# Optimization experiments

Hardware: AMD Instinct MI355X
Metric: run time of the kernel (lower is better)

The kernel has to match this reference:

```python
import jax, jax.numpy as jnp
import numpy as np
from jax.scipy.linalg import solve_triangular

B = 131072; OBS = 128; AD = 8; H = 64; FH = 32; NL = 4
D1 = AD // 2; D2 = AD - D1; TRIL = AD * (AD + 1) // 2
_rows, _cols = np.tril_indices(AD)          # same row-major order as torch.tril_indices
_diag = (_rows == _cols)                    # bool mask over TRIL entries
_diag_pos = np.where(_diag)[0]
LOG2PI = float(np.log(2.0 * np.pi))
EPS = float(np.finfo(np.float32).eps)       # torch RMSNorm default eps = finfo.eps


def _rms(x, w):
    return x * jax.lax.rsqrt(jnp.mean(x * x, axis=-1, keepdims=True) + EPS) * w


def setup_inputs() -> dict:
    ks = iter(jax.random.split(jax.random.key(0), 32))
    def w(shape, scale):
        return jax.random.normal(next(ks), shape, jnp.float32) * scale
    z = lambda *s: jnp.zeros(s, jnp.float32)
    return dict(
        x=jax.random.normal(next(ks), (B, OBS), jnp.float32),
        action=jax.random.normal(next(ks), (B, AD), jnp.float32),
        z_rpo=jax.random.uniform(next(ks), (B, AD), jnp.float32, -0.1, 0.1),
        cW1=w((OBS, H), OBS ** -0.5), cb1=z(H), c_rms=jnp.ones(H, jnp.float32),
        cW2=w((H, H), H ** -0.5), cb2=z(H), cW3=w((H, 1), H ** -0.5), cb3=z(1),
        aW1=w((OBS, H), OBS ** -0.5), ab1=z(H), aW2=w((H, H), H ** -0.5), ab2=z(H),
        mW=w((H, AD), 0.01), mb=z(AD),
        tW1=w((OBS, H), OBS ** -0.5), tb1=z(H), t_rms1=jnp.ones(H, jnp.float32),
        tW2=w((H, H), H ** -0.5), tb2=z(H), t_rms2=jnp.ones(H, jnp.float32),
        hW=w((H, TRIL), 0.01), hb=z(TRIL),
        fW1=w((NL, D1 + OBS, FH), (D1 + OBS) ** -0.5), fb1=z(NL, FH),
        fW2=w((NL, FH, 2 * D2), 0.01), fb2=z(NL, 2 * D2),
    )


def reference(x, action, z_rpo, cW1, cb1, c_rms, cW2, cb2, cW3, cb3,
              aW1, ab1, aW2, ab2, mW, mb,
              tW1, tb1, t_rms1, tW2, tb2, t_rms2, hW, hb,
              fW1, fb1, fW2, fb2):
    silu = jax.nn.silu
    Bn = x.shape[0]
    # actor mean trunk + head, with RPO uniform perturbation (action is given)
    h = silu(silu(x @ aW1 + ab1) @ aW2 + ab2)
    action_mean = h @ mW + mb + z_rpo
    # state-dependent lower-triangular covariance factor
    tl = _rms(silu(x @ tW1 + tb1), t_rms1)
    tl = _rms(silu(tl @ tW2 + tb2), t_rms2)
    raw = tl @ hW + hb                                   # [B, TRIL]
    proc = jnp.where(_diag, jax.nn.softplus(raw), raw)
    L = jnp.zeros((Bn, AD, AD), raw.dtype).at[:, _rows, _cols].set(proc)
    log_det_L = jnp.log(proc[:, _diag_pos]).sum(-1)      # [B]
    # coupling flow inverse: noise -> correlated
    noise = action - action_mean
    x1, x2 = noise[:, :D1], noise[:, D1:]
    fld = jnp.zeros((Bn,), raw.dtype)
    for i in reversed(range(NL)):
        cond, y = (x1, x2) if i % 2 == 0 else (x2, x1)
        st = silu(jnp.concatenate([cond, x], -1) @ fW1[i] + fb1[i]) @ fW2[i] + fb2[i]
        s_raw, tshift = jnp.split(st, 2, -1)
        s = jnp.tanh(s_raw) * 2.0
        xt = (y - tshift) * jnp.exp(-s)
        if i % 2 == 0:
            x2 = xt
        else:
            x1 = xt
        fld = fld + s.sum(-1)
    correlated = jnp.concatenate([x1, x2], -1)           # [B, AD]
    zc = solve_triangular(L, correlated[..., None], lower=True)[..., 0]
    mahal = (zc * zc).sum(-1)
    log_prob = -0.5 * (AD * LOG2PI + mahal) - log_det_L - fld
    entropy = 0.5 * (AD * (1.0 + LOG2PI)) + log_det_L + fld
    # critic
    v = _rms(silu(x @ cW1 + cb1), c_rms)
    v = silu(v @ cW2 + cb2) @ cW3 + cb3                  # [B, 1]
    return (action, log_prob, entropy, v)
```

## Files before the change

### kernel.cpp

```cpp
#include <hip/hip_runtime.h>

typedef __attribute__((ext_vector_type(8))) short    v8s;
typedef __attribute__((ext_vector_type(4))) float    f4;
typedef __attribute__((ext_vector_type(2))) float    f2;
typedef __attribute__((ext_vector_type(2))) unsigned u32x2;

#define MFMA16 __builtin_amdgcn_mfma_f32_16x16x32_bf16

#define AW1T 0
#define TW1T 8192
#define CW1T 16384
#define AW2T 24576
#define TW2T 28672
#define CW2T 32768
#define MWT  36864
#define HWT  37888
#define FW1XT 40960
#define FW2T  57344
#define WS_BF16_TOTAL 59392
#define W1CTO 0
#define HBPO  512

#define LOG2PI 1.83787706640934548356f
#define EPSF   1.1920928955078125e-07f

__device__ __constant__ int PERM[36] = {0,2,5,9,14,20,27,35,
  1,3,4,6,7,8,10,11,12,13,15,16,17,18,19,21,22,23,24,25,26,28,29,30,31,32,33,34};

__device__ __forceinline__ float ubits(unsigned u){union{unsigned u;float f;}c;c.u=u;return c.f;}
__device__ __forceinline__ unsigned fbits(float f){union{float f;unsigned u;}c;c.f=f;return c.u;}
__device__ __forceinline__ float rcpf(float x){ return __builtin_amdgcn_rcpf(x); }
__device__ __forceinline__ float siluf(float v){ return v * rcpf(1.f + __expf(-v)); }
__device__ __forceinline__ unsigned pk2(float a,float b){
  unsigned ua=fbits(a); ua+=0x7fffu+((ua>>16)&1u);
  unsigned ub=fbits(b); ub+=0x7fffu+((ub>>16)&1u);
  return (ua>>16)|(ub&0xffff0000u);
}
__device__ __forceinline__ unsigned short f2bu(float a){
  unsigned ua=fbits(a); ua+=0x7fffu+((ua>>16)&1u);
  return (unsigned short)(ua>>16);
}
__device__ __forceinline__ float b2f16(unsigned short h){ return ubits(((unsigned)h)<<16); }
__device__ __forceinline__ float qsum(float v){
  v += __shfl_xor(v,16,64); v += __shfl_xor(v,32,64); return v;
}
__device__ __forceinline__ int swz(int row, int blk){ return row*64 + ((blk ^ (row&7))*8); }

__global__ __launch_bounds__(256)
void prep_kernel(const float* __restrict__ aW1, const float* __restrict__ aW2,
                 const float* __restrict__ mW,  const float* __restrict__ tW1,
                 const float* __restrict__ tW2, const float* __restrict__ hW,
                 const float* __restrict__ hb,  const float* __restrict__ cW1,
                 const float* __restrict__ cW2, const float* __restrict__ fW1,
                 const float* __restrict__ fW2,
                 unsigned short* __restrict__ ws16, float* __restrict__ wsf)
{
  const int tid = blockIdx.x*256 + threadIdx.x;
  const int stride = gridDim.x*256;
  for (int idx=tid; idx<64*128; idx+=stride){
    int n=idx>>7, k=idx&127;
    ws16[AW1T+idx]=f2bu(aW1[k*64+n]);
    ws16[TW1T+idx]=f2bu(tW1[k*64+n]);
    ws16[CW1T+idx]=f2bu(cW1[k*64+n]);
  }
  for (int idx=tid; idx<64*64; idx+=stride){
    int n=idx>>6, k=idx&63;
    ws16[AW2T+idx]=f2bu(aW2[k*64+n]);
    ws16[TW2T+idx]=f2bu(tW2[k*64+n]);
    ws16[CW2T+idx]=f2bu(cW2[k*64+n]);
  }
  for (int idx=tid; idx<16*64; idx+=stride){
    int n=idx>>6, k=idx&63;
    ws16[MWT+idx]=f2bu(n<8 ? mW[k*8+n] : 0.f);
  }
  for (int idx=tid; idx<48*64; idx+=stride){
    int n=idx>>6, k=idx&63;
    ws16[HWT+idx]=f2bu(n<36 ? hW[k*36+PERM[n]] : 0.f);
  }
  for (int idx=tid; idx<4*32*128; idx+=stride){
    int i=idx>>12, rem=idx&4095, n=rem>>7, k=rem&127;
    ws16[FW1XT+idx]=f2bu(fW1[i*4224 + (4+k)*32 + n]);
  }
  for (int idx=tid; idx<4*16*32; idx+=stride){
    int i=idx>>9, rem=idx&511, n=rem>>5, k=rem&31;
    ws16[FW2T+idx]=f2bu(n<8 ? fW2[i*256 + k*8 + n] : 0.f);
  }
  for (int idx=tid; idx<4*32*4; idx+=stride){
    int i=idx>>7, rem=idx&127, n=rem>>2, k=rem&3;
    wsf[W1CTO+idx]=fW1[i*4224 + k*32 + n];
  }
  for (int idx=tid; idx<48; idx+=stride)
    wsf[HBPO+idx] = idx<36 ? hb[PERM[idx]] : 0.f;
}

template<int NWT>
__device__ __forceinline__ void gemmX(const unsigned short* __restrict__ Wt,
                                      const v8s* __restrict__ xf,
                                      f4 (*acc)[2], int c, int q)
{
#pragma unroll
  for (int kt=0; kt<4; ++kt){
    v8s wf[NWT];
#pragma unroll
    for (int wt=0; wt<NWT; ++wt)
      wf[wt] = *(const v8s*)(Wt + (wt*16 + c)*128 + kt*32 + q*8);
#pragma unroll
    for (int wt=0; wt<NWT; ++wt)
#pragma unroll
      for (int et=0; et<2; ++et)
        acc[wt][et] = MFMA16(wf[wt], xf[et*4+kt], acc[wt][et], 0,0,0);
  }
}

template<int NWT>
__device__ __forceinline__ void gemmH(const unsigned short* __restrict__ Wt,
                                      const unsigned short* __restrict__ actL,
                                      f4 (*acc)[2], int c, int q)
{
#pragma unroll
  for (int kt=0; kt<2; ++kt){
    v8s wf[NWT];
#pragma unroll
    for (int wt=0; wt<NWT; ++wt)
      wf[wt] = *(const v8s*)(Wt + (wt*16 + c)*64 + kt*32 + q*8);
    v8s af[2];
#pragma unroll
    for (int et=0; et<2; ++et)
      af[et] = *(const v8s*)(actL + swz(et*16+c, kt*4+q));
#pragma unroll
    for (int wt=0; wt<NWT; ++wt)
#pragma unroll
      for (int et=0; et<2; ++et)
        acc[wt][et] = MFMA16(wf[wt], af[et], acc[wt][et], 0,0,0);
  }
}

__global__ __launch_bounds__(64) __attribute__((amdgpu_waves_per_eu(3, 4)))
void policy_kernel(
    const float* __restrict__ x,    const float* __restrict__ action, const float* __restrict__ z_rpo,
    const float* __restrict__ cb1,  const float* __restrict__ c_rms,  const float* __restrict__ cb2,
    const float* __restrict__ cW3,  const float* __restrict__ cb3,
    const float* __restrict__ ab1,  const float* __restrict__ ab2,    const float* __restrict__ mb,
    const float* __restrict__ tb1,  const float* __restrict__ t_rms1, const float* __restrict__ tb2,
    const float* __restrict__ t_rms2,
    const float* __restrict__ fb1,  const float* __restrict__ fb2,
    const unsigned short* __restrict__ ws16, const float* __restrict__ wsf,
    float* __restrict__ out, const int Btot)
{
  const int lane = threadIdx.x;
  const int q = lane >> 4, c = lane & 15;
  const int b0 = blockIdx.x << 5;

  __shared__ alignas(16) unsigned char smem[7936];
  unsigned short* actL = (unsigned short*)smem;
  unsigned short* hidL = (unsigned short*)smem;
  unsigned short* triL = (unsigned short*)(smem + 4096);
  float*          nstL = (float*)(smem + 6400);
  unsigned short* amL  = (unsigned short*)(smem + 7424);

  v8s xf[8];
  {
    const float* xb = x + (size_t)b0*128;
#pragma unroll
    for (int et=0; et<2; ++et)
#pragma unroll
      for (int kt=0; kt<4; ++kt){
        const float* p = xb + (size_t)(et*16+c)*128 + kt*32 + q*8;
        f4 u0 = *(const f4*)p, u1 = *(const f4*)(p+4);
        union { unsigned u[4]; v8s v; } r;
        r.u[0]=pk2(u0[0],u0[1]); r.u[1]=pk2(u0[2],u0[3]);
        r.u[2]=pk2(u1[0],u1[1]); r.u[3]=pk2(u1[2],u1[3]);
        xf[et*4+kt] = r.v;
      }
  }

  f4 acc[4][2];
  const f4 z4 = {0.f,0.f,0.f,0.f};

#pragma unroll
  for (int wt=0; wt<4; ++wt) for (int et=0; et<2; ++et) acc[wt][et]=z4;
  gemmX<4>(ws16+AW1T, xf, acc, c, q);
#pragma unroll
  for (int wt=0; wt<4; ++wt){
    const f4 bv = *(const f4*)(ab1 + wt*16 + q*4);
#pragma unroll
    for (int et=0; et<2; ++et){
      float s0=siluf(acc[wt][et][0]+bv[0]), s1=siluf(acc[wt][et][1]+bv[1]);
      float s2=siluf(acc[wt][et][2]+bv[2]), s3=siluf(acc[wt][et][3]+bv[3]);
      u32x2 u = {pk2(s0,s1), pk2(s2,s3)};
      *(u32x2*)(actL + swz(et*16+c, wt*2+(q>>1)) + (q&1)*4) = u;
    }
  }
#pragma unroll
  for (int wt=0; wt<4; ++wt) for (int et=0; et<2; ++et) acc[wt][et]=z4;
  gemmH<4>(ws16+AW2T, actL, acc, c, q);
#pragma unroll
  for (int wt=0; wt<4; ++wt){
    const f4 bv = *(const f4*)(ab2 + wt*16 + q*4);
#pragma unroll
    for (int et=0; et<2; ++et){
      float s0=siluf(acc[wt][et][0]+bv[0]), s1=siluf(acc[wt][et][1]+bv[1]);
      float s2=siluf(acc[wt][et][2]+bv[2]), s3=siluf(acc[wt][et][3]+bv[3]);
      u32x2 u = {pk2(s0,s1), pk2(s2,s3)};
      *(u32x2*)(actL + swz(et*16+c, wt*2+(q>>1)) + (q&1)*4) = u;
    }
  }
  {
    f4 am1[1][2]; am1[0][0]=z4; am1[0][1]=z4;
    gemmH<1>(ws16+MWT, actL, am1, c, q);
    if (q<2){
      const f4 mbv = *(const f4*)(mb + q*4);
#pragma unroll
      for (int et=0; et<2; ++et){
        u32x2 u = {pk2(am1[0][et][0]+mbv[0], am1[0][et][1]+mbv[1]),
                   pk2(am1[0][et][2]+mbv[2], am1[0][et][3]+mbv[3])};
        *(u32x2*)(amL + (et*16+c)*8 + q*4) = u;
      }
    }
  }

#pragma unroll
  for (int wt=0; wt<4; ++wt) for (int et=0; et<2; ++et) acc[wt][et]=z4;
  gemmX<4>(ws16+TW1T, xf, acc, c, q);
  float r1[2];
  {
    float ss[2]={0.f,0.f};
#pragma unroll
    for (int wt=0; wt<4; ++wt){
      const f4 bv = *(const f4*)(tb1 + wt*16 + q*4);
      const f4 rw = *(const f4*)(t_rms1 + wt*16 + q*4);
#pragma unroll
      for (int et=0; et<2; ++et){
        float s0=siluf(acc[wt][et][0]+bv[0]), s1=siluf(acc[wt][et][1]+bv[1]);
        float s2=siluf(acc[wt][et][2]+bv[2]), s3=siluf(acc[wt][et][3]+bv[3]);
        ss[et] += s0*s0+s1*s1+s2*s2+s3*s3;
        u32x2 u = {pk2(s0*rw[0],s1*rw[1]), pk2(s2*rw[2],s3*rw[3])};
        *(u32x2*)(actL + swz(et*16+c, wt*2+(q>>1)) + (q&1)*4) = u;
      }
    }
#pragma unroll
    for (int et=0; et<2; ++et) r1[et]=rsqrtf(qsum(ss[et])*(1.f/64.f)+EPSF);
  }
#pragma unroll
  for (int wt=0; wt<4; ++wt) for (int et=0; et<2; ++et) acc[wt][et]=z4;
  gemmH<4>(ws16+TW2T, actL, acc, c, q);
  float r2[2];
  {
    float ss[2]={0.f,0.f};
#pragma unroll
    for (int wt=0; wt<4; ++wt){
      const f4 bv = *(const f4*)(tb2 + wt*16 + q*4);
      const f4 rw = *(const f4*)(t_rms2 + wt*16 + q*4);
#pragma unroll
      for (int et=0; et<2; ++et){
        float s0=siluf(r1[et]*acc[wt][et][0]+bv[0]), s1=siluf(r1[et]*acc[wt][et][1]+bv[1]);
        float s2=siluf(r1[et]*acc[wt][et][2]+bv[2]), s3=siluf(r1[et]*acc[wt][et][3]+bv[3]);
        ss[et] += s0*s0+s1*s1+s2*s2+s3*s3;
        u32x2 u = {pk2(s0*rw[0],s1*rw[1]), pk2(s2*rw[2],s3*rw[3])};
        *(u32x2*)(actL + swz(et*16+c, wt*2+(q>>1)) + (q&1)*4) = u;
      }
    }
#pragma unroll
    for (int et=0; et<2; ++et) r2[et]=rsqrtf(qsum(ss[et])*(1.f/64.f)+EPSF);
  }
  float ldet[2];
  {
    f4 a3[3][2];
#pragma unroll
    for (int wt=0; wt<3; ++wt) for (int et=0; et<2; ++et) a3[wt][et]=z4;
    gemmH<3>(ws16+HWT, actL, a3, c, q);
    float ldp[2]={0.f,0.f};
#pragma unroll
    for (int wt=0; wt<3; ++wt){
      const f4 hbv = *(const f4*)(wsf + HBPO + wt*16 + q*4);
#pragma unroll
      for (int et=0; et<2; ++et){
        float t0=r2[et]*a3[wt][et][0]+hbv[0], t1=r2[et]*a3[wt][et][1]+hbv[1];
        float t2=r2[et]*a3[wt][et][2]+hbv[2], t3=r2[et]*a3[wt][et][3]+hbv[3];
        if (wt==0 && q<2){
          t0=fmaxf(t0,0.f)+__logf(1.f+__expf(-fabsf(t0)));
          t1=fmaxf(t1,0.f)+__logf(1.f+__expf(-fabsf(t1)));
          t2=fmaxf(t2,0.f)+__logf(1.f+__expf(-fabsf(t2)));
          t3=fmaxf(t3,0.f)+__logf(1.f+__expf(-fabsf(t3)));
          ldp[et] += __logf(t0)+__logf(t1)+__logf(t2)+__logf(t3);
        }
        if (wt<2 || q==0){
          u32x2 u = {pk2(t0,t1), pk2(t2,t3)};
          *(u32x2*)(triL + (et*16+c)*36 + wt*16 + q*4) = u;
        }
      }
    }
#pragma unroll
    for (int et=0; et<2; ++et) ldet[et]=qsum(ldp[et]);
  }

#pragma unroll
  for (int wt=0; wt<4; ++wt) for (int et=0; et<2; ++et) acc[wt][et]=z4;
  gemmX<4>(ws16+CW1T, xf, acc, c, q);
  float rc[2];
  {
    float ss[2]={0.f,0.f};
#pragma unroll
    for (int wt=0; wt<4; ++wt){
      const f4 bv = *(const f4*)(cb1 + wt*16 + q*4);
      const f4 rw = *(const f4*)(c_rms + wt*16 + q*4);
#pragma unroll
      for (int et=0; et<2; ++et){
        float s0=siluf(acc[wt][et][0]+bv[0]), s1=siluf(acc[wt][et][1]+bv[1]);
        float s2=siluf(acc[wt][et][2]+bv[2]), s3=siluf(acc[wt][et][3]+bv[3]);
        ss[et] += s0*s0+s1*s1+s2*s2+s3*s3;
        u32x2 u = {pk2(s0*rw[0],s1*rw[1]), pk2(s2*rw[2],s3*rw[3])};
        *(u32x2*)(actL + swz(et*16+c, wt*2+(q>>1)) + (q&1)*4) = u;
      }
    }
#pragma unroll
    for (int et=0; et<2; ++et) rc[et]=rsqrtf(qsum(ss[et])*(1.f/64.f)+EPSF);
  }
  float vv[2];
  {
#pragma unroll
    for (int wt=0; wt<4; ++wt) for (int et=0; et<2; ++et) acc[wt][et]=z4;
    gemmH<4>(ws16+CW2T, actL, acc, c, q);
    float vp[2]={0.f,0.f};
#pragma unroll
    for (int wt=0; wt<4; ++wt){
      const f4 bv = *(const f4*)(cb2 + wt*16 + q*4);
      const f4 wv = *(const f4*)(cW3 + wt*16 + q*4);
#pragma unroll
      for (int et=0; et<2; ++et){
        vp[et] = fmaf(siluf(rc[et]*acc[wt][et][0]+bv[0]), wv[0], vp[et]);
        vp[et] = fmaf(siluf(rc[et]*acc[wt][et][1]+bv[1]), wv[1], vp[et]);
        vp[et] = fmaf(siluf(rc[et]*acc[wt][et][2]+bv[2]), wv[2], vp[et]);
        vp[et] = fmaf(siluf(rc[et]*acc[wt][et][3]+bv[3]), wv[3], vp[et]);
      }
    }
    const float cb3v = cb3[0];
#pragma unroll
    for (int et=0; et<2; ++et) vv[et]=qsum(vp[et])+cb3v;
  }

  const int l = lane;
  float nst[8], fld=0.f;
  if (l < 32){
    const size_t bb = (size_t)(b0+l)*8;
    f4 a0=*(const f4*)(action+bb), a1=*(const f4*)(action+bb+4);
    f4 zr0=*(const f4*)(z_rpo+bb), zr1=*(const f4*)(z_rpo+bb+4);
    *(f4*)(out+bb)=a0; *(f4*)(out+bb+4)=a1;
#pragma unroll
    for (int j=0;j<4;++j){
      nst[j]   = a0[j]-b2f16(amL[l*8+j])  -zr0[j];
      nst[4+j] = a1[j]-b2f16(amL[l*8+4+j])-zr1[j];
    }
    *(f4*)(nstL + l*8)     = (f4){nst[0],nst[1],nst[2],nst[3]};
    *(f4*)(nstL + l*8 + 4) = (f4){nst[4],nst[5],nst[6],nst[7]};
  }

#pragma unroll
  for (int ii=0; ii<4; ++ii){
    const int i = 3-ii;
    const int cb = (i&1)?4:0, yb = (i&1)?0:4;
    f4 a2[2][2];
#pragma unroll
    for (int wt=0; wt<2; ++wt) for (int et=0; et<2; ++et) a2[wt][et]=z4;
    gemmX<2>(ws16+FW1XT+i*4096, xf, a2, c, q);
    float nv[2][4];
#pragma unroll
    for (int et=0; et<2; ++et){
      const float* np = nstL + (et*16+c)*8 + cb;
      f2 t0=*(const f2*)np, t1=*(const f2*)(np+2);
      nv[et][0]=t0[0]; nv[et][1]=t0[1]; nv[et][2]=t1[0]; nv[et][3]=t1[1];
    }
#pragma unroll
    for (int wt=0; wt<2; ++wt){
      const f4 bv = *(const f4*)(fb1 + i*32 + wt*16 + q*4);
      float sh[2][4];
#pragma unroll
      for (int r=0; r<4; ++r){
        const f4 wc = *(const f4*)(wsf + W1CTO + i*128 + (wt*16+q*4+r)*4);
#pragma unroll
        for (int et=0; et<2; ++et){
          float hv = a2[wt][et][r] + bv[r]
                   + wc[0]*nv[et][0] + wc[1]*nv[et][1]
                   + wc[2]*nv[et][2] + wc[3]*nv[et][3];
          sh[et][r] = siluf(hv);
        }
      }
#pragma unroll
      for (int et=0; et<2; ++et){
        u32x2 u = {pk2(sh[et][0],sh[et][1]), pk2(sh[et][2],sh[et][3])};
        *(u32x2*)(hidL + swz(et*16+c, wt*2+(q>>1)) + (q&1)*4) = u;
      }
    }
    {
      const v8s wf3 = *(const v8s*)(ws16 + FW2T + i*512 + c*32 + q*8);
      f4 as[2];
#pragma unroll
      for (int et=0; et<2; ++et){
        const v8s hf = *(const v8s*)(hidL + swz(et*16+c, q));
        f4 a1s = z4;
        a1s = MFMA16(wf3, hf, a1s, 0,0,0);
        as[et]=a1s;
      }
      if (q<2){
        const f4 fbv = *(const f4*)(fb2 + i*8 + q*4);
#pragma unroll
        for (int et=0; et<2; ++et){
          u32x2 u = {pk2(as[et][0]+fbv[0], as[et][1]+fbv[1]),
                     pk2(as[et][2]+fbv[2], as[et][3]+fbv[3])};
          *(u32x2*)(amL + (et*16+c)*8 + q*4) = u;
        }
      }
    }
    if (l < 32){
      float sr0=b2f16(amL[l*8+0]), sr1=b2f16(amL[l*8+1]);
      float sr2=b2f16(amL[l*8+2]), sr3=b2f16(amL[l*8+3]);
      float th0=b2f16(amL[l*8+4]), th1=b2f16(amL[l*8+5]);
      float th2=b2f16(amL[l*8+6]), th3=b2f16(amL[l*8+7]);
      float s0=2.f-4.f*rcpf(__expf(2.f*sr0)+1.f);
      float s1=2.f-4.f*rcpf(__expf(2.f*sr1)+1.f);
      float s2=2.f-4.f*rcpf(__expf(2.f*sr2)+1.f);
      float s3=2.f-4.f*rcpf(__expf(2.f*sr3)+1.f);
      nst[yb+0]=(nst[yb+0]-th0)*__expf(-s0);
      nst[yb+1]=(nst[yb+1]-th1)*__expf(-s1);
      nst[yb+2]=(nst[yb+2]-th2)*__expf(-s2);
      nst[yb+3]=(nst[yb+3]-th3)*__expf(-s3);
      *(f4*)(nstL + l*8 + yb) = (f4){nst[yb+0],nst[yb+1],nst[yb+2],nst[yb+3]};
      fld += s0+s1+s2+s3;
    }
  }

  if (l < 32){
    constexpr int INVPERM[36] = {0,8,1,9,10,2,11,12,13,3,14,15,16,17,4,18,19,20,
                                 21,22,5,23,24,25,26,27,28,6,29,30,31,32,33,34,35,7};
    float tri[36];
#pragma unroll
    for (int j=0;j<36;++j) tri[j] = b2f16(triL[l*36 + INVPERM[j]]);
    float zv[8], mahal=0.f;
#pragma unroll
    for (int r=0;r<8;++r){
      float s=nst[r];
      const int base=(r*(r+1))>>1;
#pragma unroll
      for (int cc=0;cc<r;++cc) s -= tri[base+cc]*zv[cc];
      const float z = s*rcpf(tri[base+r]);
      zv[r]=z; mahal+=z*z;
    }
    const float ldet_s = (l<16)?ldet[0]:ldet[1];
    const float v_s    = (l<16)?vv[0]:vv[1];
    const float lp = -0.5f*(8.f*LOG2PI+mahal) - ldet_s - fld;
    const float en =  0.5f*(8.f*(1.f+LOG2PI)) + ldet_s + fld;
    out[(size_t)Btot*8  + b0 + l] = lp;
    out[(size_t)Btot*9  + b0 + l] = en;
    out[(size_t)Btot*10 + b0 + l] = v_s;
  }
}

extern "C" void kernel_launch(void* const* d_in, const int* in_sizes, int n_in,
                              void* d_out, int out_size, void* d_ws, size_t ws_size,
                              hipStream_t stream) {
  const float* x      = (const float*)d_in[0];
  const float* action = (const float*)d_in[1];
  const float* z_rpo  = (const float*)d_in[2];
  const float* cW1    = (const float*)d_in[3];
  const float* cb1    = (const float*)d_in[4];
  const float* c_rms  = (const float*)d_in[5];
  const float* cW2    = (const float*)d_in[6];
  const float* cb2    = (const float*)d_in[7];
  const float* cW3    = (const float*)d_in[8];
  const float* cb3    = (const float*)d_in[9];
  const float* aW1    = (const float*)d_in[10];
  const float* ab1    = (const float*)d_in[11];
  const float* aW2    = (const float*)d_in[12];
  const float* ab2    = (const float*)d_in[13];
  const float* mW     = (const float*)d_in[14];
  const float* mb     = (const float*)d_in[15];
  const float* tW1    = (const float*)d_in[16];
  const float* tb1    = (const float*)d_in[17];
  const float* t_rms1 = (const float*)d_in[18];
  const float* tW2    = (const float*)d_in[19];
  const float* tb2    = (const float*)d_in[20];
  const float* t_rms2 = (const float*)d_in[21];
  const float* hW     = (const float*)d_in[22];
  const float* hb     = (const float*)d_in[23];
  const float* fW1    = (const float*)d_in[24];
  const float* fb1    = (const float*)d_in[25];
  const float* fW2    = (const float*)d_in[26];
  const float* fb2    = (const float*)d_in[27];
  float* out = (float*)d_out;

  unsigned short* ws16 = (unsigned short*)d_ws;
  float* wsf = (float*)((char*)d_ws + WS_BF16_TOTAL*2);

  const int Btot = in_sizes[0] / 128;

  hipLaunchKernelGGL(prep_kernel, dim3(128), dim3(256), 0, stream,
                     aW1, aW2, mW, tW1, tW2, hW, hb, cW1, cW2, fW1, fW2, ws16, wsf);
  hipLaunchKernelGGL(policy_kernel, dim3(Btot/32), dim3(64), 0, stream,
                     x, action, z_rpo, cb1, c_rms, cb2, cW3, cb3,
                     ab1, ab2, mb, tb1, t_rms1, tb2, t_rms2, fb1, fb2,
                     ws16, wsf, out, Btot);
}
```

Measured before the change: 224.6 us.

## Pre-swizzle weights into MFMA fragment order and stage x loads through LDS

The prep kernel now writes every bf16 weight matrix in per-lane MFMA fragment order, so each wave's weight load becomes one contiguous 1 KB read instead of 16-byte pieces strided by rows. The x tile is now read with fully coalesced 64-byte-per-lane row reads, converted to bf16, written to a swizzled LDS buffer, and gathered back into fragments after a barrier. This is meant to cut global memory transactions for both weights and activations, at the cost of an extra LDS round trip, a barrier, and slightly more shared memory.

Result: faster. 191.0 us (-15.0%).

```diff
diff --git a/kernel.cpp b/kernel.cpp
--- a/kernel.cpp
+++ b/kernel.cpp
@@ -45,6 +45,7 @@
   v += __shfl_xor(v,16,64); v += __shfl_xor(v,32,64); return v;
 }
 __device__ __forceinline__ int swz(int row, int blk){ return row*64 + ((blk ^ (row&7))*8); }
+__device__ __forceinline__ int swzx(int row, int blk){ return row*128 + ((blk ^ (row&7))*8); }
 
 __global__ __launch_bounds__(256)
 void prep_kernel(const float* __restrict__ aW1, const float* __restrict__ aW2,
@@ -58,32 +59,45 @@
   const int tid = blockIdx.x*256 + threadIdx.x;
   const int stride = gridDim.x*256;
   for (int idx=tid; idx<64*128; idx+=stride){
-    int n=idx>>7, k=idx&127;
+    int f=idx>>9, r=idx&511, lane=r>>3, j=idx&7;
+    int wt=f>>2, kt=f&3, c=lane&15, q=lane>>4;
+    int n=wt*16+c, k=kt*32+q*8+j;
     ws16[AW1T+idx]=f2bu(aW1[k*64+n]);
     ws16[TW1T+idx]=f2bu(tW1[k*64+n]);
     ws16[CW1T+idx]=f2bu(cW1[k*64+n]);
   }
   for (int idx=tid; idx<64*64; idx+=stride){
-    int n=idx>>6, k=idx&63;
+    int f=idx>>9, r=idx&511, lane=r>>3, j=idx&7;
+    int wt=f>>1, kt=f&1, c=lane&15, q=lane>>4;
+    int n=wt*16+c, k=kt*32+q*8+j;
     ws16[AW2T+idx]=f2bu(aW2[k*64+n]);
     ws16[TW2T+idx]=f2bu(tW2[k*64+n]);
     ws16[CW2T+idx]=f2bu(cW2[k*64+n]);
   }
   for (int idx=tid; idx<16*64; idx+=stride){
-    int n=idx>>6, k=idx&63;
+    int f=idx>>9, r=idx&511, lane=r>>3, j=idx&7;
+    int kt=f, c=lane&15, q=lane>>4;
+    int n=c, k=kt*32+q*8+j;
     ws16[MWT+idx]=f2bu(n<8 ? mW[k*8+n] : 0.f);
   }
   for (int idx=tid; idx<48*64; idx+=stride){
-    int n=idx>>6, k=idx&63;
+    int f=idx>>9, r=idx&511, lane=r>>3, j=idx&7;
+    int wt=f>>1, kt=f&1, c=lane&15, q=lane>>4;
+    int n=wt*16+c, k=kt*32+q*8+j;
     ws16[HWT+idx]=f2bu(n<36 ? hW[k*36+PERM[n]] : 0.f);
   }
   for (int idx=tid; idx<4*32*128; idx+=stride){
-    int i=idx>>12, rem=idx&4095, n=rem>>7, k=rem&127;
+    int i=idx>>12, rem=idx&4095;
+    int f=rem>>9, r=rem&511, lane=r>>3, j=idx&7;
+    int wt=f>>2, kt=f&3, c=lane&15, q=lane>>4;
+    int n=wt*16+c, k=kt*32+q*8+j;
     ws16[FW1XT+idx]=f2bu(fW1[i*4224 + (4+k)*32 + n]);
   }
   for (int idx=tid; idx<4*16*32; idx+=stride){
-    int i=idx>>9, rem=idx&511, n=rem>>5, k=rem&31;
-    ws16[FW2T+idx]=f2bu(n<8 ? fW2[i*256 + k*8 + n] : 0.f);
+    int i=idx>>9, r=idx&511, lane=r>>3, j=idx&7;
+    int c=lane&15, q=lane>>4;
+    int k=q*8+j;
+    ws16[FW2T+idx]=f2bu(c<8 ? fW2[i*256 + k*8 + c] : 0.f);
   }
   for (int idx=tid; idx<4*32*4; idx+=stride){
     int i=idx>>7, rem=idx&127, n=rem>>2, k=rem&3;
@@ -96,14 +110,14 @@
 template<int NWT>
 __device__ __forceinline__ void gemmX(const unsigned short* __restrict__ Wt,
                                       const v8s* __restrict__ xf,
-                                      f4 (*acc)[2], int c, int q)
+                                      f4 (*acc)[2], int lane)
 {
 #pragma unroll
   for (int kt=0; kt<4; ++kt){
     v8s wf[NWT];
 #pragma unroll
     for (int wt=0; wt<NWT; ++wt)
-      wf[wt] = *(const v8s*)(Wt + (wt*16 + c)*128 + kt*32 + q*8);
+      wf[wt] = *(const v8s*)(Wt + ((wt*4 + kt)*64 + lane)*8);
 #pragma unroll
     for (int wt=0; wt<NWT; ++wt)
 #pragma unroll
@@ -115,14 +129,14 @@
 template<int NWT>
 __device__ __forceinline__ void gemmH(const unsigned short* __restrict__ Wt,
                                       const unsigned short* __restrict__ actL,
-                                      f4 (*acc)[2], int c, int q)
+                                      f4 (*acc)[2], int lane, int c, int q)
 {
 #pragma unroll
   for (int kt=0; kt<2; ++kt){
     v8s wf[NWT];
 #pragma unroll
     for (int wt=0; wt<NWT; ++wt)
-      wf[wt] = *(const v8s*)(Wt + (wt*16 + c)*64 + kt*32 + q*8);
+      wf[wt] = *(const v8s*)(Wt + ((wt*2 + kt)*64 + lane)*8);
     v8s af[2];
 #pragma unroll
     for (int et=0; et<2; ++et)
@@ -151,27 +165,37 @@
   const int q = lane >> 4, c = lane & 15;
   const int b0 = blockIdx.x << 5;
 
-  __shared__ alignas(16) unsigned char smem[7936];
+  __shared__ alignas(16) unsigned char smem[8192];
   unsigned short* actL = (unsigned short*)smem;
   unsigned short* hidL = (unsigned short*)smem;
   unsigned short* triL = (unsigned short*)(smem + 4096);
   float*          nstL = (float*)(smem + 6400);
   unsigned short* amL  = (unsigned short*)(smem + 7424);
+  unsigned short* xL   = (unsigned short*)smem;
 
   v8s xf[8];
   {
     const float* xb = x + (size_t)b0*128;
+    const int rr = lane>>3, bb = (lane&7)*2;
+#pragma unroll
+    for (int rg=0; rg<4; ++rg){
+      const int row = rg*8 + rr;
+      const float* p = xb + row*128 + (lane&7)*16;
+      f4 u0=*(const f4*)p, u1=*(const f4*)(p+4), u2=*(const f4*)(p+8), u3=*(const f4*)(p+12);
+      union { unsigned u[4]; v8s v; } r0, r1;
+      r0.u[0]=pk2(u0[0],u0[1]); r0.u[1]=pk2(u0[2],u0[3]);
+      r0.u[2]=pk2(u1[0],u1[1]); r0.u[3]=pk2(u1[2],u1[3]);
+      r1.u[0]=pk2(u2[0],u2[1]); r1.u[1]=pk2(u2[2],u2[3]);
+      r1.u[2]=pk2(u3[0],u3[1]); r1.u[3]=pk2(u3[2],u3[3]);
+      *(v8s*)(xL + swzx(row, bb  )) = r0.v;
+      *(v8s*)(xL + swzx(row, bb+1)) = r1.v;
+    }
+    __syncthreads();
 #pragma unroll
     for (int et=0; et<2; ++et)
 #pragma unroll
-      for (int kt=0; kt<4; ++kt){
-        const float* p = xb + (size_t)(et*16+c)*128 + kt*32 + q*8;
-        f4 u0 = *(const f4*)p, u1 = *(const f4*)(p+4);
-        union { unsigned u[4]; v8s v; } r;
-        r.u[0]=pk2(u0[0],u0[1]); r.u[1]=pk2(u0[2],u0[3]);
-        r.u[2]=pk2(u1[0],u1[1]); r.u[3]=pk2(u1[2],u1[3]);
-        xf[et*4+kt] = r.v;
-      }
+      for (int kt=0; kt<4; ++kt)
+        xf[et*4+kt] = *(const v8s*)(xL + swzx(et*16+c, kt*4+q));
   }
 
   f4 acc[4][2];
@@ -179,7 +203,7 @@
 
 #pragma unroll
   for (int wt=0; wt<4; ++wt) for (int et=0; et<2; ++et) acc[wt][et]=z4;
-  gemmX<4>(ws16+AW1T, xf, acc, c, q);
+  gemmX<4>(ws16+AW1T, xf, acc, lane);
 #pragma unroll
   for (int wt=0; wt<4; ++wt){
     const f4 bv = *(const f4*)(ab1 + wt*16 + q*4);
@@ -193,7 +217,7 @@
   }
 #pragma unroll
   for (int wt=0; wt<4; ++wt) for (int et=0; et<2; ++et) acc[wt][et]=z4;
-  gemmH<4>(ws16+AW2T, actL, acc, c, q);
+  gemmH<4>(ws16+AW2T, actL, acc, lane, c, q);
 #pragma unroll
   for (int wt=0; wt<4; ++wt){
     const f4 bv = *(const f4*)(ab2 + wt*16 + q*4);
@@ -207,7 +231,7 @@
   }
   {
     f4 am1[1][2]; am1[0][0]=z4; am1[0][1]=z4;
-    gemmH<1>(ws16+MWT, actL, am1, c, q);
+    gemmH<1>(ws16+MWT, actL, am1, lane, c, q);
     if (q<2){
       const f4 mbv = *(const f4*)(mb + q*4);
 #pragma unroll
@@ -221,7 +245,7 @@
 
 #pragma unroll
   for (int wt=0; wt<4; ++wt) for (int et=0; et<2; ++et) acc[wt][et]=z4;
-  gemmX<4>(ws16+TW1T, xf, acc, c, q);
+  gemmX<4>(ws16+TW1T, xf, acc, lane);
   float r1[2];
   {
     float ss[2]={0.f,0.f};
@@ -243,7 +267,7 @@
   }
 #pragma unroll
   for (int wt=0; wt<4; ++wt) for (int et=0; et<2; ++et) acc[wt][et]=z4;
-  gemmH<4>(ws16+TW2T, actL, acc, c, q);
+  gemmH<4>(ws16+TW2T, actL, acc, lane, c, q);
   float r2[2];
   {
     float ss[2]={0.f,0.f};
@@ -268,7 +292,7 @@
     f4 a3[3][2];
 #pragma unroll
     for (int wt=0; wt<3; ++wt) for (int et=0; et<2; ++et) a3[wt][et]=z4;
-    gemmH<3>(ws16+HWT, actL, a3, c, q);
+    gemmH<3>(ws16+HWT, actL, a3, lane, c, q);
     float ldp[2]={0.f,0.f};
 #pragma unroll
     for (int wt=0; wt<3; ++wt){
@@ -296,7 +320,7 @@
 
 #pragma unroll
   for (int wt=0; wt<4; ++wt) for (int et=0; et<2; ++et) acc[wt][et]=z4;
-  gemmX<4>(ws16+CW1T, xf, acc, c, q);
+  gemmX<4>(ws16+CW1T, xf, acc, lane);
   float rc[2];
   {
     float ss[2]={0.f,0.f};
@@ -320,7 +344,7 @@
   {
 #pragma unroll
     for (int wt=0; wt<4; ++wt) for (int et=0; et<2; ++et) acc[wt][et]=z4;
-    gemmH<4>(ws16+CW2T, actL, acc, c, q);
+    gemmH<4>(ws16+CW2T, actL, acc, lane, c, q);
     float vp[2]={0.f,0.f};
 #pragma unroll
     for (int wt=0; wt<4; ++wt){
@@ -362,7 +386,7 @@
     f4 a2[2][2];
 #pragma unroll
     for (int wt=0; wt<2; ++wt) for (int et=0; et<2; ++et) a2[wt][et]=z4;
-    gemmX<2>(ws16+FW1XT+i*4096, xf, a2, c, q);
+    gemmX<2>(ws16+FW1XT+i*4096, xf, a2, lane);
     float nv[2][4];
 #pragma unroll
     for (int et=0; et<2; ++et){
@@ -392,7 +416,7 @@
       }
     }
     {
-      const v8s wf3 = *(const v8s*)(ws16 + FW2T + i*512 + c*32 + q*8);
+      const v8s wf3 = *(const v8s*)(ws16 + FW2T + i*512 + lane*8);
       f4 as[2];
 #pragma unroll
       for (int et=0; et<2; ++et){
```
